# Optimization experiments

Hardware: AMD Instinct MI355X
Metric: run time of the kernel (lower is better)

Reference implementation:

```python
import jax, jax.numpy as jnp
import numpy as np

SCORE_THRESHOLD = 0.01
NMS_THRESHOLD = 0.5
MAX_DETECTIONS = 100
PRE_NMS_TOPK = 200  # candidates kept per class before NMS (>= MAX_DETECTIONS)


def setup_inputs() -> dict:
    key = jax.random.key(0)
    kc, kcls, kw, kr, kt = jax.random.split(key, 5)
    B, N, C, R = 16, 100000, 30, 3
    # Build valid (x1,y1,x2,y2) boxes: random centers in a 512x512 image, sizes in [1,101].
    cxy = jax.random.uniform(kc, (B, N, 2), dtype=jnp.float32) * 512.0
    wh = jax.random.uniform(kw, (B, N, 2), dtype=jnp.float32) * 100.0 + 1.0
    boxes = jnp.concatenate([cxy - 0.5 * wh, cxy + 0.5 * wh], axis=-1)  # [B,N,4]
    classification = jax.random.uniform(kcls, (B, N, C), dtype=jnp.float32)
    rotation = jax.random.normal(kr, (B, N, R), dtype=jnp.float32)
    translation = jax.random.normal(kt, (B, N, 3), dtype=jnp.float32)
    return {"boxes": boxes, "classification": classification,
            "rotation": rotation, "translation": translation}


def _iou_matrix(b):  # b: [K,4] -> [K,K] pairwise IoU
    x1, y1, x2, y2 = b[:, 0], b[:, 1], b[:, 2], b[:, 3]
    area = jnp.maximum(x2 - x1, 0.0) * jnp.maximum(y2 - y1, 0.0)
    xx1 = jnp.maximum(x1[:, None], x1[None, :])
    yy1 = jnp.maximum(y1[:, None], y1[None, :])
    xx2 = jnp.minimum(x2[:, None], x2[None, :])
    yy2 = jnp.minimum(y2[:, None], y2[None, :])
    inter = jnp.maximum(xx2 - xx1, 0.0) * jnp.maximum(yy2 - yy1, 0.0)
    union = area[:, None] + area[None, :] - inter
    return inter / jnp.maximum(union, 1e-8)


def _nms_one_class(scores, boxes):
    # scores: [N], boxes: [N,4] -> (kept_scores [K], source_indices [K])
    masked = jnp.where(scores > SCORE_THRESHOLD, scores, -jnp.inf)
    top_s, top_i = jax.lax.top_k(masked, PRE_NMS_TOPK)
    cand = boxes[top_i]                      # [K,4], already sorted by score desc
    iou = _iou_matrix(cand)                  # [K,K]
    valid = jnp.isfinite(top_s)
    rng = jnp.arange(PRE_NMS_TOPK)

    def body(i, keep):
        suppress = (iou[i] > NMS_THRESHOLD) & (rng > i) & keep[i]
        return keep & ~suppress

    keep = jax.lax.fori_loop(0, PRE_NMS_TOPK, body, valid)
    return jnp.where(keep, top_s, -jnp.inf), top_i


def reference(boxes, classification, rotation, translation):
    B, N, C = classification.shape

    def per_image(bx, cls, rot, tr):
        # Per-class score threshold + NMS, vectorized over classes.
        s, idx = jax.vmap(lambda c: _nms_one_class(cls[:, c], bx))(jnp.arange(C))
        labels = jnp.broadcast_to(jnp.arange(C)[:, None], s.shape)
        s, idx, labels = s.reshape(-1), idx.reshape(-1), labels.reshape(-1)
        # Global top-k over all (class, kept-box) pairs.
        top_s, sel = jax.lax.top_k(s, MAX_DETECTIONS)
        fidx, flab = idx[sel], labels[sel]
        valid = jnp.isfinite(top_s)
        out_boxes = jnp.where(valid[:, None], bx[fidx], -1.0)
        out_scores = jnp.where(valid, top_s, -1.0)
        out_labels = jnp.where(valid, flab, -1).astype(jnp.int32)
        out_rot = jnp.where(valid[:, None], rot[fidx], -1.0)
        out_tr = jnp.where(valid[:, None], tr[fidx], -1.0)
        return out_boxes, out_scores, out_labels, out_rot, out_tr

    return jax.vmap(per_image)(boxes, classification, rotation, translation)
```

## Files before the change

kernel.cpp:

```cpp
#include <hip/hip_runtime.h>
#include <math.h>

typedef unsigned long long u64;

#define BATCH 16
#define NBOX 100000
#define NCLS 30
#define K 200
#define MAXDET 100
#define SCORE_THR 0.01f
#define NMS_THR 0.5f
#define T0 0.995f

#define ELEM_PER_BATCH (NBOX * NCLS)
#define CAP 1024
#define CHUNKS 48
#define VEC_PER_CHUNK 15625
#define SEG 48
#define OVF 1000000

#define OFF_COLL   0ull
#define OFF_PCNT   (OFF_COLL + (size_t)BATCH*NCLS*CHUNKS*SEG*8)
#define OFF_WSI    (OFF_PCNT + (size_t)BATCH*CHUNKS*32*4)
#define OFF_MERGE  (OFF_WSI + (size_t)BATCH*NCLS*K*4)

__global__ __launch_bounds__(512) void collect_kernel(const float* __restrict__ cls,
                                                      int* __restrict__ pcnt,
                                                      u64* __restrict__ coll) {
  const int b = blockIdx.x / CHUNKS;
  const int chunk = blockIdx.x % CHUNKS;
  const int tid = threadIdx.x;

  __shared__ u64 lbuf[NCLS][SEG];
  __shared__ int lcnt[NCLS];

  if (tid < NCLS) lcnt[tid] = 0;
  __syncthreads();

  const int vbase = chunk * VEC_PER_CHUNK;
  const float4* p = (const float4*)(cls + (size_t)b * ELEM_PER_BATCH) + vbase;

  auto process = [&](float4 v, int idx) {
    float m = fmaxf(fmaxf(v.x, v.y), fmaxf(v.z, v.w));
    if (m > T0) {
      float vv[4] = {v.x, v.y, v.z, v.w};
      #pragma unroll
      for (int j = 0; j < 4; ++j) {
        if (vv[j] > T0) {
          int e = (vbase + idx) * 4 + j;
          int c = e % NCLS;
          int n = e / NCLS;
          int pos = atomicAdd(&lcnt[c], 1);
          if (pos < SEG)
            lbuf[c][pos] = ((u64)__float_as_uint(vv[j]) << 32) | (unsigned)(~(unsigned)n);
        }
      }
    }
  };

  int i = tid;
  for (; i + 1536 < VEC_PER_CHUNK; i += 2048) {
    float4 a  = p[i];
    float4 b2 = p[i + 512];
    float4 c2 = p[i + 1024];
    float4 d2 = p[i + 1536];
    process(a,  i);
    process(b2, i + 512);
    process(c2, i + 1024);
    process(d2, i + 1536);
  }
  for (; i < VEC_PER_CHUNK; i += 512) process(p[i], i);
  __syncthreads();

  if (tid < NCLS) {
    int m = lcnt[tid];
    pcnt[(b * CHUNKS + chunk) * 32 + tid] = (m > SEG) ? OVF : m;
    lcnt[tid] = (m < SEG) ? m : SEG;
  }
  __syncthreads();

  for (int t = tid; t < NCLS * SEG; t += 512) {
    int c = t / SEG, s = t - (t / SEG) * SEG;
    if (s < lcnt[c])
      coll[((size_t)(b * NCLS + c) * CHUNKS + chunk) * SEG + s] = lbuf[c][s];
  }
}

__global__ __launch_bounds__(512) void fused_sort_nms_kernel(
    const u64* __restrict__ coll, const int* __restrict__ pcnt,
    const float* __restrict__ cls, const float* __restrict__ boxes,
    int* __restrict__ ws_i, u64* __restrict__ merged) {
  const int bc = blockIdx.x;
  const int b = bc / NCLS, c = bc % NCLS;
  const int tid = threadIdx.x;

  __shared__ u64 arr[CAP];
  __shared__ u64 arr2[CAP];
  __shared__ float sx1[K], sy1[K], sx2[K], sy2[K], sarea[K], ss[K];
  __shared__ int sidx[K];
  __shared__ unsigned mask[K][8];
  __shared__ unsigned keepw[8];
  __shared__ int s_surv;
  __shared__ u64 comb[256];
  __shared__ unsigned eqbuf[512];
  __shared__ unsigned s_pref, s_mask, s_krem, s_takeall;
  __shared__ unsigned s_cntgt, s_cnteq;
  __shared__ int scnt[CHUNKS], soff[CHUNKS];
  __shared__ int s_total, s_bad;

  if (tid < CHUNKS) scnt[tid] = pcnt[(b * CHUNKS + tid) * 32 + c];
  __syncthreads();
  if (tid == 0) {
    int tot = 0, bad = 0;
    for (int ch = 0; ch < CHUNKS; ++ch) {
      int v = scnt[ch];
      if (v > SEG) bad = 1;
      soff[ch] = tot;
      tot += v;
    }
    if (tot < K || tot > CAP) bad = 1;
    s_total = tot; s_bad = bad;
  }
  __syncthreads();
  const bool bad = (s_bad != 0);

  if (!bad) {
    const int N = (s_total <= 512) ? 512 : CAP;
    for (int i = tid; i < N; i += 512) arr[i] = 0ull;
    __syncthreads();
    for (int t = tid; t < CHUNKS * SEG; t += 512) {
      int ch = t / SEG, s = t - (t / SEG) * SEG;
      if (s < scnt[ch])
        arr[soff[ch] + s] = coll[((size_t)bc * CHUNKS + ch) * SEG + s];
    }
    __syncthreads();

    {
      const int lane = tid & 63, w = tid >> 6;
      for (int run = w; run < (N >> 6); run += 8) {
        u64 v = arr[(run << 6) + lane];
        #pragma unroll
        for (int k = 2; k <= 64; k <<= 1) {
          #pragma unroll
          for (int j = k >> 1; j > 0; j >>= 1) {
            u64 o = __shfl_xor(v, j, 64);
            bool up = ((lane & k) == 0);
            bool lower = ((lane & j) == 0);
            u64 mn = (v < o) ? v : o;
            u64 mx = (v < o) ? o : v;
            v = (up != lower) ? mn : mx;
          }
        }
        arr[(run << 6) + lane] = v;
      }
    }
    __syncthreads();

    u64* src = arr;
    u64* dst = arr2;
    for (int L = 64; L < N; L <<= 1) {
      const int twoL = L << 1;
      for (int t = tid; t < N; t += 512) {
        int pair = t / twoL;
        int diag = t - pair * twoL;
        const u64* A = src + pair * twoL;
        const u64* B = A + L;
        int lo = (diag > L) ? (diag - L) : 0;
        int hi = (diag < L) ? diag : L;
        while (lo < hi) {
          int mid = (lo + hi) >> 1;
          if (A[mid] >= B[diag - 1 - mid]) lo = mid + 1; else hi = mid;
        }
        int i2 = lo, j2 = diag - lo;
        u64 av = (i2 < L) ? A[i2] : 0ull;
        u64 bv = (j2 < L) ? B[j2] : 0ull;
        dst[t] = (i2 < L && (j2 >= L || av >= bv)) ? av : bv;
      }
      __syncthreads();
      u64* tmp = src; src = dst; dst = tmp;
    }

    for (int r = tid; r < K; r += 512) {
      u64 e = src[r];
      float s = (e != 0ull) ? __uint_as_float((unsigned)(e >> 32)) : -INFINITY;
      int idx = (e != 0ull) ? (int)(~(unsigned)e) : 0;
      ss[r] = s; sidx[r] = idx;
      ws_i[bc * K + r] = idx;
    }
  } else {
    unsigned (*hist)[256] = (unsigned (*)[256])arr;
    const int wv = tid >> 6;
    if (tid == 0) { s_pref = 0u; s_mask = 0u; s_krem = K; s_takeall = 0u; }
    __syncthreads();
    const float* col = cls + (size_t)b * NBOX * NCLS + c;

    for (int pass = 0; pass < 4; ++pass) {
      if (s_takeall) break;
      const int shift = 24 - 8 * pass;
      for (int i = tid; i < 8 * 256; i += 512) ((unsigned*)hist)[i] = 0u;
      __syncthreads();
      const unsigned pref = s_pref, msk = s_mask;
      for (int n = tid; n < NBOX; n += 512) {
        float v = col[(size_t)n * NCLS];
        if (v > SCORE_THR) {
          unsigned key = __float_as_uint(v);
          if ((key & msk) == pref)
            atomicAdd(&hist[wv][(key >> shift) & 0xFFu], 1u);
        }
      }
      __syncthreads();
      if (tid < 256) {
        unsigned t2 = 0;
        for (int w = 0; w < 8; ++w) t2 += hist[w][tid];
        hist[0][tid] = t2;
      }
      __syncthreads();
      if (tid == 0) {
        unsigned krem = s_krem, cum = 0; int dsel = -1;
        for (int d = 255; d >= 0; --d) {
          unsigned cc = hist[0][d];
          if (cum + cc >= krem) { dsel = d; break; }
          cum += cc;
        }
        if (dsel < 0) s_takeall = 1u;
        else {
          s_krem = krem - cum;
          s_pref = pref | ((unsigned)dsel << shift);
          s_mask = msk | (0xFFu << shift);
        }
      }
      __syncthreads();
    }

    if (tid == 0) { s_cntgt = 0u; s_cnteq = 0u; }
    __syncthreads();
    const unsigned pivot = s_pref;
    const unsigned takeall = s_takeall;

    for (int n = tid; n < NBOX; n += 512) {
      float v = col[(size_t)n * NCLS];
      if (v > SCORE_THR) {
        unsigned key = __float_as_uint(v);
        if (takeall || key > pivot) {
          unsigned pos = atomicAdd(&s_cntgt, 1u);
          if (pos < 256u)
            comb[pos] = ((u64)key << 32) | (unsigned)(~(unsigned)n);
        } else if (key == pivot) {
          unsigned pos = atomicAdd(&s_cnteq, 1u);
          if (pos < 512u) eqbuf[pos] = (unsigned)n;
        }
      }
    }
    __syncthreads();
    const unsigned cntgt = (s_cntgt < 256u) ? s_cntgt : 256u;
    const unsigned cnteq = (s_cnteq < 512u) ? s_cnteq : 512u;
    unsigned need = 0;
    if (!takeall) {
      need = (cntgt < (unsigned)K) ? ((unsigned)K - cntgt) : 0u;
      if (need > cnteq) need = cnteq;
    }
    for (int i = tid; i < 512; i += 512)
      if ((unsigned)i >= cnteq) eqbuf[i] = 0xFFFFFFFFu;
    for (int k = 2; k <= 512; k <<= 1) {
      for (int j = k >> 1; j > 0; j >>= 1) {
        __syncthreads();
        {
          int i = tid, l = i ^ j;
          if (l > i) {
            unsigned a = eqbuf[i], bb = eqbuf[l];
            bool up = ((i & k) == 0);
            if (up ? (a > bb) : (a < bb)) { eqbuf[i] = bb; eqbuf[l] = a; }
          }
        }
      }
    }
    __syncthreads();
    for (int t = tid; t < (int)need; t += 512)
      comb[cntgt + t] = ((u64)pivot << 32) | (unsigned)(~eqbuf[t]);
    const unsigned M = cntgt + need;
    for (int i = tid; i < 256; i += 512)
      if ((unsigned)i >= M) comb[i] = 0ull;
    for (int k = 2; k <= 256; k <<= 1) {
      for (int j = k >> 1; j > 0; j >>= 1) {
        __syncthreads();
        if (tid < 256) {
          int i = tid, l = i ^ j;
          if (l > i) {
            u64 a = comb[i], bb = comb[l];
            bool up = ((i & k) == 0);
            if (up ? (a < bb) : (a > bb)) { comb[i] = bb; comb[l] = a; }
          }
        }
      }
    }
    __syncthreads();
    if (tid < K) {
      if ((unsigned)tid < M) {
        u64 e = comb[tid];
        ss[tid] = __uint_as_float((unsigned)(e >> 32));
        sidx[tid] = (int)(~(unsigned)e);
      } else {
        ss[tid] = -INFINITY;
        sidx[tid] = 0;
      }
      ws_i[bc * K + tid] = sidx[tid];
    }
  }
  for (int i = tid; i < K * 8; i += 512) ((unsigned*)mask)[i] = 0u;
  if (tid < 8) keepw[tid] = 0u;
  __syncthreads();

  for (int r = tid; r < K; r += 512) {
    float s = ss[r];
    bool valid = (s != -INFINITY);
    float x1 = 0.f, y1 = 0.f, x2 = 0.f, y2 = 0.f;
    if (valid) {
      const float* bp = boxes + ((size_t)b * NBOX + sidx[r]) * 4;
      x1 = bp[0]; y1 = bp[1]; x2 = bp[2]; y2 = bp[3];
      atomicOr(&keepw[r >> 5], 1u << (r & 31));
    }
    sx1[r] = x1; sy1[r] = y1; sx2[r] = x2; sy2[r] = y2;
    sarea[r] = fmaxf(x2 - x1, 0.f) * fmaxf(y2 - y1, 0.f);
  }
  __syncthreads();

  for (int t = tid; t < K * K; t += 512) {
    int i = t / K, j = t - i * K;
    if (j > i) {
      float xx1 = fmaxf(sx1[i], sx1[j]);
      float yy1 = fmaxf(sy1[i], sy1[j]);
      float xx2 = fminf(sx2[i], sx2[j]);
      float yy2 = fminf(sy2[i], sy2[j]);
      float inter = fmaxf(xx2 - xx1, 0.f) * fmaxf(yy2 - yy1, 0.f);
      float uni = sarea[i] + sarea[j] - inter;
      float iou = inter / fmaxf(uni, 1e-8f);
      if (iou > NMS_THR) atomicOr(&mask[i][j >> 5], 1u << (j & 31));
    }
  }
  __syncthreads();

  if (tid < 64) {
    int w = tid & 7;
    unsigned keep = keepw[w];
    for (int i = 0; i < K; ++i) {
      unsigned kw = __shfl(keep, i >> 5, 64);
      if ((kw >> (i & 31)) & 1u)
        keep &= ~mask[i][w];
    }
    if (tid < 8) keepw[tid] = keep;
  }
  __syncthreads();

  for (int r = tid; r < K; r += 512) {
    int w6 = r >> 5, bit = r & 31;
    if ((keepw[w6] >> bit) & 1u) {
      int pos = 0;
      #pragma unroll
      for (int w = 0; w < 7; ++w) {
        unsigned kw = keepw[w];
        if (w < w6) pos += __popc(kw);
        else if (w == w6) pos += __popc(kw & ((1u << bit) - 1u));
      }
      if (pos < 128) {
        unsigned ord = __float_as_uint(ss[r]) | 0x80000000u;
        merged[((size_t)b * 32 + c) * 128 + pos] =
          ((u64)ord << 32) | (unsigned)(~(unsigned)(c * K + r));
      }
    }
  }
  if (tid == 0) {
    int S = 0;
    #pragma unroll
    for (int w = 0; w < 7; ++w) S += __popc(keepw[w]);
    s_surv = S;
  }
  __syncthreads();
  for (int t = s_surv + tid; t < 128; t += 512)
    merged[((size_t)b * 32 + c) * 128 + t] = 0ull;
}

__device__ __forceinline__ int merge_path_128(const u64* __restrict__ A,
                                              const u64* __restrict__ B, int diag) {
  int lo = 0, hi = diag;
  while (lo < hi) {
    int mid = (lo + hi) >> 1;
    if (A[mid] >= B[diag - 1 - mid]) lo = mid + 1; else hi = mid;
  }
  return lo;
}

__global__ __launch_bounds__(1024) void merge_gather_kernel(
    const u64* __restrict__ merged, const int* __restrict__ ws_i,
    const float* __restrict__ boxes, const float* __restrict__ rot,
    const float* __restrict__ tr, float* __restrict__ out) {
  const int b = blockIdx.x;
  const int tid = threadIdx.x;
  __shared__ u64 S0[32 * 128];
  __shared__ u64 S1[16 * 128];

  for (int t = tid; t < 4096; t += 1024) {
    int c = t >> 7, r = t & 127;
    S0[t] = (c < NCLS) ? merged[((size_t)b * 32 + c) * 128 + r] : 0ull;
  }
  __syncthreads();

  #pragma unroll
  for (int level = 0; level < 5; ++level) {
    const int npairs = 16 >> level;
    const int nout = npairs * 128;
    const u64* src = (level & 1) ? S1 : S0;
    u64* dst = (level & 1) ? S0 : S1;
    for (int t = tid; t < nout; t += 1024) {
      int p = t >> 7, r = t & 127;
      const u64* A = src + (2 * p) * 128;
      const u64* B = src + (2 * p + 1) * 128;
      int i = merge_path_128(A, B, r);
      int j = r - i;
      u64 a = A[i], bb = B[j];
      dst[p * 128 + r] = (a >= bb) ? a : bb;
    }
    __syncthreads();
  }

  if (tid < MAXDET) {
    u64 key = S1[tid];
    bool valid = (key != 0ull);
    float* ob  = out + ((size_t)b * MAXDET + tid) * 4;
    float* os  = out + (size_t)BATCH * MAXDET * 4 + b * MAXDET + tid;
    float* ol  = os + BATCH * MAXDET;
    float* orr = out + (size_t)BATCH * MAXDET * 6 + ((size_t)b * MAXDET + tid) * 3;
    float* ot  = orr + (size_t)BATCH * MAXDET * 3;

    if (valid) {
      unsigned f = ~(unsigned)key;
      int cl = (int)(f / K);
      float sc = __uint_as_float((unsigned)(key >> 32) & 0x7FFFFFFFu);
      int orig = ws_i[(size_t)b * NCLS * K + f];
      const float* bp = boxes + ((size_t)b * NBOX + orig) * 4;
      ob[0] = bp[0]; ob[1] = bp[1]; ob[2] = bp[2]; ob[3] = bp[3];
      *os = sc;
      *ol = (float)cl;
      const float* rp = rot + ((size_t)b * NBOX + orig) * 3;
      orr[0] = rp[0]; orr[1] = rp[1]; orr[2] = rp[2];
      const float* tp = tr + ((size_t)b * NBOX + orig) * 3;
      ot[0] = tp[0]; ot[1] = tp[1]; ot[2] = tp[2];
    } else {
      ob[0] = ob[1] = ob[2] = ob[3] = -1.f;
      *os = -1.f; *ol = -1.f;
      orr[0] = orr[1] = orr[2] = -1.f;
      ot[0] = ot[1] = ot[2] = -1.f;
    }
  }
}

extern "C" void kernel_launch(void* const* d_in, const int* in_sizes, int n_in,
                              void* d_out, int out_size, void* d_ws, size_t ws_size,
                              hipStream_t stream) {
  const float* boxes = (const float*)d_in[0];
  const float* cls   = (const float*)d_in[1];
  const float* rot   = (const float*)d_in[2];
  const float* tr    = (const float*)d_in[3];
  float* out = (float*)d_out;

  char* ws = (char*)d_ws;
  u64*   coll   = (u64*)(ws + OFF_COLL);
  int*   pcnt   = (int*)(ws + OFF_PCNT);
  int*   ws_i   = (int*)(ws + OFF_WSI);
  u64*   merged = (u64*)(ws + OFF_MERGE);

  collect_kernel<<<BATCH * CHUNKS, 512, 0, stream>>>(cls, pcnt, coll);
  fused_sort_nms_kernel<<<BATCH * NCLS, 512, 0, stream>>>(coll, pcnt, cls, boxes,
                                                          ws_i, merged);
  merge_gather_kernel<<<BATCH, 1024, 0, stream>>>(merged, ws_i, boxes, rot, tr, out);
}
```

Before: 92.98 us.

## Fuse three kernels into one cooperative kernel with grid-wide syncs

Merges the collect, per-class sort+NMS, and final merge/gather kernels into a single cooperative kernel of BATCH*NCLS blocks, separated by grid.sync() barriers. The collect phase is re-chunked to 30 chunks of 25000 vectors with 64-entry segments so the collect grid matches the per-class block count. This is meant to remove kernel launch gaps and inter-kernel drain. In exchange it adds grid-barrier cost, caps occupancy through launch bounds, and gives the collect phase fewer, larger blocks.

```diff
diff --git a/kernel.cpp b/kernel.cpp
--- a/kernel.cpp
+++ b/kernel.cpp
@@ -1,6 +1,8 @@
 #include <hip/hip_runtime.h>
+#include <hip/hip_cooperative_groups.h>
 #include <math.h>
 
+namespace cg = cooperative_groups;
 typedef unsigned long long u64;
 
 #define BATCH 16
@@ -14,88 +16,28 @@
 
 #define ELEM_PER_BATCH (NBOX * NCLS)
 #define CAP 1024
-#define CHUNKS 48
-#define VEC_PER_CHUNK 15625
-#define SEG 48
+#define CHUNKS 30
+#define VEC_PER_CHUNK 25000
+#define SEG 64
 #define OVF 1000000
+#define NBLK (BATCH * NCLS)
 
 #define OFF_COLL   0ull
-#define OFF_PCNT   (OFF_COLL + (size_t)BATCH*NCLS*CHUNKS*SEG*8)
-#define OFF_WSI    (OFF_PCNT + (size_t)BATCH*CHUNKS*32*4)
-#define OFF_MERGE  (OFF_WSI + (size_t)BATCH*NCLS*K*4)
-
-__global__ __launch_bounds__(512) void collect_kernel(const float* __restrict__ cls,
-                                                      int* __restrict__ pcnt,
-                                                      u64* __restrict__ coll) {
-  const int b = blockIdx.x / CHUNKS;
-  const int chunk = blockIdx.x % CHUNKS;
+#define OFF_PCNT   (OFF_COLL + (size_t)NBLK*CHUNKS*SEG*8)
+#define OFF_WSI    (OFF_PCNT + (size_t)NBLK*32*4)
+#define OFF_MERGE  (OFF_WSI + (size_t)NBLK*K*4)
+
+__global__ __launch_bounds__(512, 4) void mega_kernel(
+    const float* __restrict__ cls, const float* __restrict__ boxes,
+    const float* __restrict__ rot, const float* __restrict__ tr,
+    int* __restrict__ pcnt, u64* __restrict__ coll,
+    int* __restrict__ ws_i, u64* __restrict__ merged, float* __restrict__ out) {
+  cg::grid_group grid = cg::this_grid();
+  const int blk = blockIdx.x;
   const int tid = threadIdx.x;
 
-  __shared__ u64 lbuf[NCLS][SEG];
-  __shared__ int lcnt[NCLS];
-
-  if (tid < NCLS) lcnt[tid] = 0;
-  __syncthreads();
-
-  const int vbase = chunk * VEC_PER_CHUNK;
-  const float4* p = (const float4*)(cls + (size_t)b * ELEM_PER_BATCH) + vbase;
-
-  auto process = [&](float4 v, int idx) {
-    float m = fmaxf(fmaxf(v.x, v.y), fmaxf(v.z, v.w));
-    if (m > T0) {
-      float vv[4] = {v.x, v.y, v.z, v.w};
-      #pragma unroll
-      for (int j = 0; j < 4; ++j) {
-        if (vv[j] > T0) {
-          int e = (vbase + idx) * 4 + j;
-          int c = e % NCLS;
-          int n = e / NCLS;
-          int pos = atomicAdd(&lcnt[c], 1);
-          if (pos < SEG)
-            lbuf[c][pos] = ((u64)__float_as_uint(vv[j]) << 32) | (unsigned)(~(unsigned)n);
-        }
-      }
-    }
-  };
-
-  int i = tid;
-  for (; i + 1536 < VEC_PER_CHUNK; i += 2048) {
-    float4 a  = p[i];
-    float4 b2 = p[i + 512];
-    float4 c2 = p[i + 1024];
-    float4 d2 = p[i + 1536];
-    process(a,  i);
-    process(b2, i + 512);
-    process(c2, i + 1024);
-    process(d2, i + 1536);
-  }
-  for (; i < VEC_PER_CHUNK; i += 512) process(p[i], i);
-  __syncthreads();
-
-  if (tid < NCLS) {
-    int m = lcnt[tid];
-    pcnt[(b * CHUNKS + chunk) * 32 + tid] = (m > SEG) ? OVF : m;
-    lcnt[tid] = (m < SEG) ? m : SEG;
-  }
-  __syncthreads();
-
-  for (int t = tid; t < NCLS * SEG; t += 512) {
-    int c = t / SEG, s = t - (t / SEG) * SEG;
-    if (s < lcnt[c])
-      coll[((size_t)(b * NCLS + c) * CHUNKS + chunk) * SEG + s] = lbuf[c][s];
-  }
-}
-
-__global__ __launch_bounds__(512) void fused_sort_nms_kernel(
-    const u64* __restrict__ coll, const int* __restrict__ pcnt,
-    const float* __restrict__ cls, const float* __restrict__ boxes,
-    int* __restrict__ ws_i, u64* __restrict__ merged) {
-  const int bc = blockIdx.x;
-  const int b = bc / NCLS, c = bc % NCLS;
-  const int tid = threadIdx.x;
-
-  __shared__ u64 arr[CAP];
-  __shared__ u64 arr2[CAP];
+  __shared__ u64 bufA[4096];
+  __shared__ u64 S1[2048];
   __shared__ float sx1[K], sy1[K], sx2[K], sy2[K], sarea[K], ss[K];
   __shared__ int sidx[K];
   __shared__ unsigned mask[K][8];
@@ -105,350 +47,405 @@
   __shared__ unsigned eqbuf[512];
   __shared__ unsigned s_pref, s_mask, s_krem, s_takeall;
   __shared__ unsigned s_cntgt, s_cnteq;
+  __shared__ int lcnt[NCLS];
   __shared__ int scnt[CHUNKS], soff[CHUNKS];
   __shared__ int s_total, s_bad;
 
-  if (tid < CHUNKS) scnt[tid] = pcnt[(b * CHUNKS + tid) * 32 + c];
-  __syncthreads();
-  if (tid == 0) {
-    int tot = 0, bad = 0;
-    for (int ch = 0; ch < CHUNKS; ++ch) {
-      int v = scnt[ch];
-      if (v > SEG) bad = 1;
-      soff[ch] = tot;
-      tot += v;
-    }
-    if (tot < K || tot > CAP) bad = 1;
-    s_total = tot; s_bad = bad;
+  {
+    const int b = blk / CHUNKS, chunk = blk % CHUNKS;
+    u64 (*lbuf)[SEG] = (u64 (*)[SEG])bufA;
+
+    if (tid < NCLS) lcnt[tid] = 0;
+    __syncthreads();
+
+    const int vbase = chunk * VEC_PER_CHUNK;
+    const float4* p = (const float4*)(cls + (size_t)b * ELEM_PER_BATCH) + vbase;
+
+    auto process = [&](float4 v, int idx) {
+      float m = fmaxf(fmaxf(v.x, v.y), fmaxf(v.z, v.w));
+      if (m > T0) {
+        float vv[4] = {v.x, v.y, v.z, v.w};
+        #pragma unroll
+        for (int j = 0; j < 4; ++j) {
+          if (vv[j] > T0) {
+            int e = (vbase + idx) * 4 + j;
+            int c = e % NCLS;
+            int n = e / NCLS;
+            int pos = atomicAdd(&lcnt[c], 1);
+            if (pos < SEG)
+              lbuf[c][pos] = ((u64)__float_as_uint(vv[j]) << 32) | (unsigned)(~(unsigned)n);
+          }
+        }
+      }
+    };
+
+    int i = tid;
+    for (; i + 1536 < VEC_PER_CHUNK; i += 2048) {
+      float4 a  = p[i];
+      float4 b2 = p[i + 512];
+      float4 c2 = p[i + 1024];
+      float4 d2 = p[i + 1536];
+      process(a,  i);
+      process(b2, i + 512);
+      process(c2, i + 1024);
+      process(d2, i + 1536);
+    }
+    for (; i < VEC_PER_CHUNK; i += 512) process(p[i], i);
+    __syncthreads();
+
+    if (tid < NCLS) {
+      int m = lcnt[tid];
+      pcnt[(b * CHUNKS + chunk) * 32 + tid] = (m > SEG) ? OVF : m;
+      lcnt[tid] = (m < SEG) ? m : SEG;
+    }
+    __syncthreads();
+
+    for (int t = tid; t < NCLS * SEG; t += 512) {
+      int c = t >> 6, s = t & (SEG - 1);
+      if (s < lcnt[c])
+        coll[((size_t)(b * NCLS + c) * CHUNKS + chunk) * SEG + s] = lbuf[c][s];
+    }
   }
-  __syncthreads();
-  const bool bad = (s_bad != 0);
-
-  if (!bad) {
-    const int N = (s_total <= 512) ? 512 : CAP;
-    for (int i = tid; i < N; i += 512) arr[i] = 0ull;
-    __syncthreads();
-    for (int t = tid; t < CHUNKS * SEG; t += 512) {
-      int ch = t / SEG, s = t - (t / SEG) * SEG;
-      if (s < scnt[ch])
-        arr[soff[ch] + s] = coll[((size_t)bc * CHUNKS + ch) * SEG + s];
-    }
-    __syncthreads();
-
-    {
-      const int lane = tid & 63, w = tid >> 6;
-      for (int run = w; run < (N >> 6); run += 8) {
-        u64 v = arr[(run << 6) + lane];
-        #pragma unroll
-        for (int k = 2; k <= 64; k <<= 1) {
+  grid.sync();
+
+  {
+    const int bc = blk;
+    const int b = bc / NCLS, c = bc % NCLS;
+    u64* arr  = bufA;
+    u64* arr2 = bufA + 1024;
+
+    if (tid < CHUNKS) scnt[tid] = pcnt[(b * CHUNKS + tid) * 32 + c];
+    __syncthreads();
+    if (tid == 0) {
+      int tot = 0, bad = 0;
+      for (int ch = 0; ch < CHUNKS; ++ch) {
+        int v = scnt[ch];
+        if (v > SEG) bad = 1;
+        soff[ch] = tot;
+        tot += v;
+      }
+      if (tot < K || tot > CAP) bad = 1;
+      s_total = tot; s_bad = bad;
+    }
+    __syncthreads();
+    const bool bad = (s_bad != 0);
+
+    if (!bad) {
+      const int N = (s_total <= 512) ? 512 : CAP;
+      for (int i = tid; i < N; i += 512) arr[i] = 0ull;
+      __syncthreads();
+      for (int t = tid; t < CHUNKS * SEG; t += 512) {
+        int ch = t >> 6, s = t & (SEG - 1);
+        if (s < scnt[ch])
+          arr[soff[ch] + s] = coll[((size_t)bc * CHUNKS + ch) * SEG + s];
+      }
+      __syncthreads();
+
+      {
+        const int lane = tid & 63, w = tid >> 6;
+        for (int run = w; run < (N >> 6); run += 8) {
+          u64 v = arr[(run << 6) + lane];
           #pragma unroll
-          for (int j = k >> 1; j > 0; j >>= 1) {
-            u64 o = __shfl_xor(v, j, 64);
-            bool up = ((lane & k) == 0);
-            bool lower = ((lane & j) == 0);
-            u64 mn = (v < o) ? v : o;
-            u64 mx = (v < o) ? o : v;
-            v = (up != lower) ? mn : mx;
-          }
-        }
-        arr[(run << 6) + lane] = v;
-      }
-    }
-    __syncthreads();
-
-    u64* src = arr;
-    u64* dst = arr2;
-    for (int L = 64; L < N; L <<= 1) {
-      const int twoL = L << 1;
-      for (int t = tid; t < N; t += 512) {
-        int pair = t / twoL;
-        int diag = t - pair * twoL;
-        const u64* A = src + pair * twoL;
-        const u64* B = A + L;
-        int lo = (diag > L) ? (diag - L) : 0;
-        int hi = (diag < L) ? diag : L;
-        while (lo < hi) {
-          int mid = (lo + hi) >> 1;
-          if (A[mid] >= B[diag - 1 - mid]) lo = mid + 1; else hi = mid;
-        }
-        int i2 = lo, j2 = diag - lo;
-        u64 av = (i2 < L) ? A[i2] : 0ull;
-        u64 bv = (j2 < L) ? B[j2] : 0ull;
-        dst[t] = (i2 < L && (j2 >= L || av >= bv)) ? av : bv;
-      }
-      __syncthreads();
-      u64* tmp = src; src = dst; dst = tmp;
-    }
-
-    for (int r = tid; r < K; r += 512) {
-      u64 e = src[r];
-      float s = (e != 0ull) ? __uint_as_float((unsigned)(e >> 32)) : -INFINITY;
-      int idx = (e != 0ull) ? (int)(~(unsigned)e) : 0;
-      ss[r] = s; sidx[r] = idx;
-      ws_i[bc * K + r] = idx;
-    }
-  } else {
-    unsigned (*hist)[256] = (unsigned (*)[256])arr;
-    const int wv = tid >> 6;
-    if (tid == 0) { s_pref = 0u; s_mask = 0u; s_krem = K; s_takeall = 0u; }
-    __syncthreads();
-    const float* col = cls + (size_t)b * NBOX * NCLS + c;
-
-    for (int pass = 0; pass < 4; ++pass) {
-      if (s_takeall) break;
-      const int shift = 24 - 8 * pass;
-      for (int i = tid; i < 8 * 256; i += 512) ((unsigned*)hist)[i] = 0u;
-      __syncthreads();
-      const unsigned pref = s_pref, msk = s_mask;
+          for (int k = 2; k <= 64; k <<= 1) {
+            #pragma unroll
+            for (int j = k >> 1; j > 0; j >>= 1) {
+              u64 o = __shfl_xor(v, j, 64);
+              bool up = ((lane & k) == 0);
+              bool lower = ((lane & j) == 0);
+              u64 mn = (v < o) ? v : o;
+              u64 mx = (v < o) ? o : v;
+              v = (up != lower) ? mn : mx;
+            }
+          }
+          arr[(run << 6) + lane] = v;
+        }
+      }
+      __syncthreads();
+
+      u64* src = arr;
+      u64* dst = arr2;
+      for (int L = 64; L < N; L <<= 1) {
+        const int twoL = L << 1;
+        for (int t = tid; t < N; t += 512) {
+          int pair = t / twoL;
+          int diag = t - pair * twoL;
+          const u64* A = src + pair * twoL;
+          const u64* B = A + L;
+          int lo = (diag > L) ? (diag - L) : 0;
+          int hi = (diag < L) ? diag : L;
+          while (lo < hi) {
+            int mid = (lo + hi) >> 1;
+            if (A[mid] >= B[diag - 1 - mid]) lo = mid + 1; else hi = mid;
+          }
+          int i2 = lo, j2 = diag - lo;
+          u64 av = (i2 < L) ? A[i2] : 0ull;
+          u64 bv = (j2 < L) ? B[j2] : 0ull;
+          dst[t] = (i2 < L && (j2 >= L || av >= bv)) ? av : bv;
+        }
+        __syncthreads();
+        u64* tmp = src; src = dst; dst = tmp;
+      }
+
+      for (int r = tid; r < K; r += 512) {
+        u64 e = src[r];
+        float s = (e != 0ull) ? __uint_as_float((unsigned)(e >> 32)) : -INFINITY;
+        int idx = (e != 0ull) ? (int)(~(unsigned)e) : 0;
+        ss[r] = s; sidx[r] = idx;
+        ws_i[bc * K + r] = idx;
+      }
+    } else {
+      unsigned (*hist)[256] = (unsigned (*)[256])bufA;
+      const int wv = tid >> 6;
+      if (tid == 0) { s_pref = 0u; s_mask = 0u; s_krem = K; s_takeall = 0u; }
+      __syncthreads();
+      const float* col = cls + (size_t)b * NBOX * NCLS + c;
+
+      for (int pass = 0; pass < 4; ++pass) {
+        if (s_takeall) break;
+        const int shift = 24 - 8 * pass;
+        for (int i = tid; i < 8 * 256; i += 512) ((unsigned*)hist)[i] = 0u;
+        __syncthreads();
+        const unsigned pref = s_pref, msk = s_mask;
+        for (int n = tid; n < NBOX; n += 512) {
+          float v = col[(size_t)n * NCLS];
+          if (v > SCORE_THR) {
+            unsigned key = __float_as_uint(v);
+            if ((key & msk) == pref)
+              atomicAdd(&hist[wv][(key >> shift) & 0xFFu], 1u);
+          }
+        }
+        __syncthreads();
+        if (tid < 256) {
+          unsigned t2 = 0;
+          for (int w = 0; w < 8; ++w) t2 += hist[w][tid];
+          hist[0][tid] = t2;
+        }
+        __syncthreads();
+        if (tid == 0) {
+          unsigned krem = s_krem, cum = 0; int dsel = -1;
+          for (int d = 255; d >= 0; --d) {
+            unsigned cc = hist[0][d];
+            if (cum + cc >= krem) { dsel = d; break; }
+            cum += cc;
+          }
+          if (dsel < 0) s_takeall = 1u;
+          else {
+            s_krem = krem - cum;
+            s_pref = pref | ((unsigned)dsel << shift);
+            s_mask = msk | (0xFFu << shift);
+          }
+        }
+        __syncthreads();
+      }
+
+      if (tid == 0) { s_cntgt = 0u; s_cnteq = 0u; }
+      __syncthreads();
+      const unsigned pivot = s_pref;
+      const unsigned takeall = s_takeall;
+
       for (int n = tid; n < NBOX; n += 512) {
         float v = col[(size_t)n * NCLS];
         if (v > SCORE_THR) {
           unsigned key = __float_as_uint(v);
-          if ((key & msk) == pref)
-            atomicAdd(&hist[wv][(key >> shift) & 0xFFu], 1u);
-        }
-      }
-      __syncthreads();
-      if (tid < 256) {
-        unsigned t2 = 0;
-        for (int w = 0; w < 8; ++w) t2 += hist[w][tid];
-        hist[0][tid] = t2;
-      }
-      __syncthreads();
-      if (tid == 0) {
-        unsigned krem = s_krem, cum = 0; int dsel = -1;
-        for (int d = 255; d >= 0; --d) {
-          unsigned cc = hist[0][d];
-          if (cum + cc >= krem) { dsel = d; break; }
-          cum += cc;
-        }
-        if (dsel < 0) s_takeall = 1u;
-        else {
-          s_krem = krem - cum;
-          s_pref = pref | ((unsigned)dsel << shift);
-          s_mask = msk | (0xFFu << shift);
-        }
-      }
-      __syncthreads();
-    }
-
-    if (tid == 0) { s_cntgt = 0u; s_cnteq = 0u; }
-    __syncthreads();
-    const unsigned pivot = s_pref;
-    const unsigned takeall = s_takeall;
-
-    for (int n = tid; n < NBOX; n += 512) {
-      float v = col[(size_t)n * NCLS];
-      if (v > SCORE_THR) {
-        unsigned key = __float_as_uint(v);
-        if (takeall || key > pivot) {
-          unsigned pos = atomicAdd(&s_cntgt, 1u);
-          if (pos < 256u)
-            comb[pos] = ((u64)key << 32) | (unsigned)(~(unsigned)n);
-        } else if (key == pivot) {
-          unsigned pos = atomicAdd(&s_cnteq, 1u);
-          if (pos < 512u) eqbuf[pos] = (unsigned)n;
-        }
-      }
-    }
-    __syncthreads();
-    const unsigned cntgt = (s_cntgt < 256u) ? s_cntgt : 256u;
-    const unsigned cnteq = (s_cnteq < 512u) ? s_cnteq : 512u;
-    unsigned need = 0;
-    if (!takeall) {
-      need = (cntgt < (unsigned)K) ? ((unsigned)K - cntgt) : 0u;
-      if (need > cnteq) need = cnteq;
-    }
-    for (int i = tid; i < 512; i += 512)
-      if ((unsigned)i >= cnteq) eqbuf[i] = 0xFFFFFFFFu;
-    for (int k = 2; k <= 512; k <<= 1) {
-      for (int j = k >> 1; j > 0; j >>= 1) {
-        __syncthreads();
-        {
-          int i = tid, l = i ^ j;
-          if (l > i) {
-            unsigned a = eqbuf[i], bb = eqbuf[l];
-            bool up = ((i & k) == 0);
-            if (up ? (a > bb) : (a < bb)) { eqbuf[i] = bb; eqbuf[l] = a; }
-          }
-        }
-      }
-    }
-    __syncthreads();
-    for (int t = tid; t < (int)need; t += 512)
-      comb[cntgt + t] = ((u64)pivot << 32) | (unsigned)(~eqbuf[t]);
-    const unsigned M = cntgt + need;
-    for (int i = tid; i < 256; i += 512)
-      if ((unsigned)i >= M) comb[i] = 0ull;
-    for (int k = 2; k <= 256; k <<= 1) {
-      for (int j = k >> 1; j > 0; j >>= 1) {
-        __syncthreads();
-        if (tid < 256) {
-          int i = tid, l = i ^ j;
-          if (l > i) {
-            u64 a = comb[i], bb = comb[l];
-            bool up = ((i & k) == 0);
-            if (up ? (a < bb) : (a > bb)) { comb[i] = bb; comb[l] = a; }
-          }
-        }
-      }
-    }
-    __syncthreads();
-    if (tid < K) {
-      if ((unsigned)tid < M) {
-        u64 e = comb[tid];
-        ss[tid] = __uint_as_float((unsigned)(e >> 32));
-        sidx[tid] = (int)(~(unsigned)e);
+          if (takeall || key > pivot) {
+            unsigned pos = atomicAdd(&s_cntgt, 1u);
+            if (pos < 256u)
+              comb[pos] = ((u64)key << 32) | (unsigned)(~(unsigned)n);
+          } else if (key == pivot) {
+            unsigned pos = atomicAdd(&s_cnteq, 1u);
+            if (pos < 512u) eqbuf[pos] = (unsigned)n;
+          }
+        }
+      }
+      __syncthreads();
+      const unsigned cntgt = (s_cntgt < 256u) ? s_cntgt : 256u;
+      const unsigned cnteq = (s_cnteq < 512u) ? s_cnteq : 512u;
+      unsigned need = 0;
+      if (!takeall) {
+        need = (cntgt < (unsigned)K) ? ((unsigned)K - cntgt) : 0u;
+        if (need > cnteq) need = cnteq;
+      }
+      for (int i = tid; i < 512; i += 512)
+        if ((unsigned)i >= cnteq) eqbuf[i] = 0xFFFFFFFFu;
+      for (int k = 2; k <= 512; k <<= 1) {
+        for (int j = k >> 1; j > 0; j >>= 1) {
+          __syncthreads();
+          {
+            int i = tid, l = i ^ j;
+            if (l > i) {
+              unsigned a = eqbuf[i], bb = eqbuf[l];
+              bool up = ((i & k) == 0);
+              if (up ? (a > bb) : (a < bb)) { eqbuf[i] = bb; eqbuf[l] = a; }
+            }
+          }
+        }
+      }
+      __syncthreads();
+      for (int t = tid; t < (int)need; t += 512)
+        comb[cntgt + t] = ((u64)pivot << 32) | (unsigned)(~eqbuf[t]);
+      const unsigned M = cntgt + need;
+      for (int i = tid; i < 256; i += 512)
+        if ((unsigned)i >= M) comb[i] = 0ull;
+      for (int k = 2; k <= 256; k <<= 1) {
+        for (int j = k >> 1; j > 0; j >>= 1) {
+          __syncthreads();
+          if (tid < 256) {
+            int i = tid, l = i ^ j;
+            if (l > i) {
+              u64 a = comb[i], bb = comb[l];
+              bool up = ((i & k) == 0);
+              if (up ? (a < bb) : (a > bb)) { comb[i] = bb; comb[l] = a; }
+            }
+          }
+        }
+      }
+      __syncthreads();
+      if (tid < K) {
+        if ((unsigned)tid < M) {
+          u64 e = comb[tid];
+          ss[tid] = __uint_as_float((unsigned)(e >> 32));
+          sidx[tid] = (int)(~(unsigned)e);
+        } else {
+          ss[tid] = -INFINITY;
+          sidx[tid] = 0;
+        }
+        ws_i[bc * K + tid] = sidx[tid];
+      }
+    }
+    for (int i = tid; i < K * 8; i += 512) ((unsigned*)mask)[i] = 0u;
+    if (tid < 8) keepw[tid] = 0u;
+    __syncthreads();
+
+    for (int r = tid; r < K; r += 512) {
+      float s = ss[r];
+      bool valid = (s != -INFINITY);
+      float x1 = 0.f, y1 = 0.f, x2 = 0.f, y2 = 0.f;
+      if (valid) {
+        const float* bp = boxes + ((size_t)b * NBOX + sidx[r]) * 4;
+        x1 = bp[0]; y1 = bp[1]; x2 = bp[2]; y2 = bp[3];
+        atomicOr(&keepw[r >> 5], 1u << (r & 31));
+      }
+      sx1[r] = x1; sy1[r] = y1; sx2[r] = x2; sy2[r] = y2;
+      sarea[r] = fmaxf(x2 - x1, 0.f) * fmaxf(y2 - y1, 0.f);
+    }
+    __syncthreads();
+
+    for (int t = tid; t < K * K; t += 512) {
+      int i = t / K, j = t - i * K;
+      if (j > i) {
+        float xx1 = fmaxf(sx1[i], sx1[j]);
+        float yy1 = fmaxf(sy1[i], sy1[j]);
+        float xx2 = fminf(sx2[i], sx2[j]);
+        float yy2 = fminf(sy2[i], sy2[j]);
+        float inter = fmaxf(xx2 - xx1, 0.f) * fmaxf(yy2 - yy1, 0.f);
+        float uni = sarea[i] + sarea[j] - inter;
+        float iou = inter / fmaxf(uni, 1e-8f);
+        if (iou > NMS_THR) atomicOr(&mask[i][j >> 5], 1u << (j & 31));
+      }
+    }
+    __syncthreads();
+
+    if (tid < 64) {
+      int w = tid & 7;
+      unsigned keep = keepw[w];
+      for (int i = 0; i < K; ++i) {
+        unsigned kw = __shfl(keep, i >> 5, 64);
+        if ((kw >> (i & 31)) & 1u)
+          keep &= ~mask[i][w];
+      }
+      if (tid < 8) keepw[tid] = keep;
+    }
+    __syncthreads();
+
+    for (int r = tid; r < K; r += 512) {
+      int w6 = r >> 5, bit = r & 31;
+      if ((keepw[w6] >> bit) & 1u) {
+        int pos = 0;
+        #pragma unroll
+        for (int w = 0; w < 7; ++w) {
+          unsigned kw = keepw[w];
+          if (w < w6) pos += __popc(kw);
+          else if (w == w6) pos += __popc(kw & ((1u << bit) - 1u));
+        }
+        if (pos < 128) {
+          unsigned ord = __float_as_uint(ss[r]) | 0x80000000u;
+          merged[((size_t)b * 32 + c) * 128 + pos] =
+            ((u64)ord << 32) | (unsigned)(~(unsigned)(c * K + r));
+        }
+      }
+    }
+    if (tid == 0) {
+      int S = 0;
+      #pragma unroll
+      for (int w = 0; w < 7; ++w) S += __popc(keepw[w]);
+      s_surv = S;
+    }
+    __syncthreads();
+    for (int t = s_surv + tid; t < 128; t += 512)
+      merged[((size_t)b * 32 + c) * 128 + t] = 0ull;
+  }
+  grid.sync();
+
+  if (blk < BATCH) {
+    const int b = blk;
+    u64* S0 = bufA;
+
+    for (int t = tid; t < 4096; t += 512) {
+      int c = t >> 7, r = t & 127;
+      S0[t] = (c < NCLS) ? merged[((size_t)b * 32 + c) * 128 + r] : 0ull;
+    }
+    __syncthreads();
+
+    #pragma unroll
+    for (int level = 0; level < 5; ++level) {
+      const int npairs = 16 >> level;
+      const int nout = npairs * 128;
+      const u64* src = (level & 1) ? S1 : S0;
+      u64* dst = (level & 1) ? S0 : S1;
+      for (int t = tid; t < nout; t += 512) {
+        int p = t >> 7, r = t & 127;
+        const u64* A = src + (2 * p) * 128;
+        const u64* B = src + (2 * p + 1) * 128;
+        int lo = 0, hi = r;
+        while (lo < hi) {
+          int mid = (lo + hi) >> 1;
+          if (A[mid] >= B[r - 1 - mid]) lo = mid + 1; else hi = mid;
+        }
+        int i = lo, j = r - i;
+        u64 a = A[i], bb = B[j];
+        dst[p * 128 + r] = (a >= bb) ? a : bb;
+      }
+      __syncthreads();
+    }
+
+    if (tid < MAXDET) {
+      u64 key = S1[tid];
+      bool valid = (key != 0ull);
+      float* ob  = out + ((size_t)b * MAXDET + tid) * 4;
+      float* os  = out + (size_t)BATCH * MAXDET * 4 + b * MAXDET + tid;
+      float* ol  = os + BATCH * MAXDET;
+      float* orr = out + (size_t)BATCH * MAXDET * 6 + ((size_t)b * MAXDET + tid) * 3;
+      float* ot  = orr + (size_t)BATCH * MAXDET * 3;
+
+      if (valid) {
+        unsigned f = ~(unsigned)key;
+        int cl = (int)(f / K);
+        float sc = __uint_as_float((unsigned)(key >> 32) & 0x7FFFFFFFu);
+        int orig = ws_i[(size_t)b * NCLS * K + f];
+        const float* bp = boxes + ((size_t)b * NBOX + orig) * 4;
+        ob[0] = bp[0]; ob[1] = bp[1]; ob[2] = bp[2]; ob[3] = bp[3];
+        *os = sc;
+        *ol = (float)cl;
+        const float* rp = rot + ((size_t)b * NBOX + orig) * 3;
+        orr[0] = rp[0]; orr[1] = rp[1]; orr[2] = rp[2];
+        const float* tp = tr + ((size_t)b * NBOX + orig) * 3;
+        ot[0] = tp[0]; ot[1] = tp[1]; ot[2] = tp[2];
       } else {
-        ss[tid] = -INFINITY;
-        sidx[tid] = 0;
-      }
-      ws_i[bc * K + tid] = sidx[tid];
-    }
-  }
-  for (int i = tid; i < K * 8; i += 512) ((unsigned*)mask)[i] = 0u;
-  if (tid < 8) keepw[tid] = 0u;
-  __syncthreads();
-
-  for (int r = tid; r < K; r += 512) {
-    float s = ss[r];
-    bool valid = (s != -INFINITY);
-    float x1 = 0.f, y1 = 0.f, x2 = 0.f, y2 = 0.f;
-    if (valid) {
-      const float* bp = boxes + ((size_t)b * NBOX + sidx[r]) * 4;
-      x1 = bp[0]; y1 = bp[1]; x2 = bp[2]; y2 = bp[3];
-      atomicOr(&keepw[r >> 5], 1u << (r & 31));
-    }
-    sx1[r] = x1; sy1[r] = y1; sx2[r] = x2; sy2[r] = y2;
-    sarea[r] = fmaxf(x2 - x1, 0.f) * fmaxf(y2 - y1, 0.f);
-  }
-  __syncthreads();
-
-  for (int t = tid; t < K * K; t += 512) {
-    int i = t / K, j = t - i * K;
-    if (j > i) {
-      float xx1 = fmaxf(sx1[i], sx1[j]);
-      float yy1 = fmaxf(sy1[i], sy1[j]);
-      float xx2 = fminf(sx2[i], sx2[j]);
-      float yy2 = fminf(sy2[i], sy2[j]);
-      float inter = fmaxf(xx2 - xx1, 0.f) * fmaxf(yy2 - yy1, 0.f);
-      float uni = sarea[i] + sarea[j] - inter;
-      float iou = inter / fmaxf(uni, 1e-8f);
-      if (iou > NMS_THR) atomicOr(&mask[i][j >> 5], 1u << (j & 31));
-    }
-  }
-  __syncthreads();
-
-  if (tid < 64) {
-    int w = tid & 7;
-    unsigned keep = keepw[w];
-    for (int i = 0; i < K; ++i) {
-      unsigned kw = __shfl(keep, i >> 5, 64);
-      if ((kw >> (i & 31)) & 1u)
-        keep &= ~mask[i][w];
-    }
-    if (tid < 8) keepw[tid] = keep;
-  }
-  __syncthreads();
-
-  for (int r = tid; r < K; r += 512) {
-    int w6 = r >> 5, bit = r & 31;
-    if ((keepw[w6] >> bit) & 1u) {
-      int pos = 0;
-      #pragma unroll
-      for (int w = 0; w < 7; ++w) {
-        unsigned kw = keepw[w];
-        if (w < w6) pos += __popc(kw);
-        else if (w == w6) pos += __popc(kw & ((1u << bit) - 1u));
-      }
-      if (pos < 128) {
-        unsigned ord = __float_as_uint(ss[r]) | 0x80000000u;
-        merged[((size_t)b * 32 + c) * 128 + pos] =
-          ((u64)ord << 32) | (unsigned)(~(unsigned)(c * K + r));
-      }
-    }
-  }
-  if (tid == 0) {
-    int S = 0;
-    #pragma unroll
-    for (int w = 0; w < 7; ++w) S += __popc(keepw[w]);
-    s_surv = S;
-  }
-  __syncthreads();
-  for (int t = s_surv + tid; t < 128; t += 512)
-    merged[((size_t)b * 32 + c) * 128 + t] = 0ull;
-}
-
-__device__ __forceinline__ int merge_path_128(const u64* __restrict__ A,
-                                              const u64* __restrict__ B, int diag) {
-  int lo = 0, hi = diag;
-  while (lo < hi) {
-    int mid = (lo + hi) >> 1;
-    if (A[mid] >= B[diag - 1 - mid]) lo = mid + 1; else hi = mid;
-  }
-  return lo;
-}
-
-__global__ __launch_bounds__(1024) void merge_gather_kernel(
-    const u64* __restrict__ merged, const int* __restrict__ ws_i,
-    const float* __restrict__ boxes, const float* __restrict__ rot,
-    const float* __restrict__ tr, float* __restrict__ out) {
-  const int b = blockIdx.x;
-  const int tid = threadIdx.x;
-  __shared__ u64 S0[32 * 128];
-  __shared__ u64 S1[16 * 128];
-
-  for (int t = tid; t < 4096; t += 1024) {
-    int c = t >> 7, r = t & 127;
-    S0[t] = (c < NCLS) ? merged[((size_t)b * 32 + c) * 128 + r] : 0ull;
-  }
-  __syncthreads();
-
-  #pragma unroll
-  for (int level = 0; level < 5; ++level) {
-    const int npairs = 16 >> level;
-    const int nout = npairs * 128;
-    const u64* src = (level & 1) ? S1 : S0;
-    u64* dst = (level & 1) ? S0 : S1;
-    for (int t = tid; t < nout; t += 1024) {
-      int p = t >> 7, r = t & 127;
-      const u64* A = src + (2 * p) * 128;
-      const u64* B = src + (2 * p + 1) * 128;
-      int i = merge_path_128(A, B, r);
-      int j = r - i;
-      u64 a = A[i], bb = B[j];
-      dst[p * 128 + r] = (a >= bb) ? a : bb;
-    }
-    __syncthreads();
-  }
-
-  if (tid < MAXDET) {
-    u64 key = S1[tid];
-    bool valid = (key != 0ull);
-    float* ob  = out + ((size_t)b * MAXDET + tid) * 4;
-    float* os  = out + (size_t)BATCH * MAXDET * 4 + b * MAXDET + tid;
-    float* ol  = os + BATCH * MAXDET;
-    float* orr = out + (size_t)BATCH * MAXDET * 6 + ((size_t)b * MAXDET + tid) * 3;
-    float* ot  = orr + (size_t)BATCH * MAXDET * 3;
-
-    if (valid) {
-      unsigned f = ~(unsigned)key;
-      int cl = (int)(f / K);
-      float sc = __uint_as_float((unsigned)(key >> 32) & 0x7FFFFFFFu);
-      int orig = ws_i[(size_t)b * NCLS * K + f];
-      const float* bp = boxes + ((size_t)b * NBOX + orig) * 4;
-      ob[0] = bp[0]; ob[1] = bp[1]; ob[2] = bp[2]; ob[3] = bp[3];
-      *os = sc;
-      *ol = (float)cl;
-      const float* rp = rot + ((size_t)b * NBOX + orig) * 3;
-      orr[0] = rp[0]; orr[1] = rp[1]; orr[2] = rp[2];
-      const float* tp = tr + ((size_t)b * NBOX + orig) * 3;
-      ot[0] = tp[0]; ot[1] = tp[1]; ot[2] = tp[2];
-    } else {
-      ob[0] = ob[1] = ob[2] = ob[3] = -1.f;
-      *os = -1.f; *ol = -1.f;
-      orr[0] = orr[1] = orr[2] = -1.f;
-      ot[0] = ot[1] = ot[2] = -1.f;
+        ob[0] = ob[1] = ob[2] = ob[3] = -1.f;
+        *os = -1.f; *ol = -1.f;
+        orr[0] = orr[1] = orr[2] = -1.f;
+        ot[0] = ot[1] = ot[2] = -1.f;
+      }
     }
   }
 }
@@ -463,13 +460,14 @@
   float* out = (float*)d_out;
 
   char* ws = (char*)d_ws;
-  u64*   coll   = (u64*)(ws + OFF_COLL);
-  int*   pcnt   = (int*)(ws + OFF_PCNT);
-  int*   ws_i   = (int*)(ws + OFF_WSI);
-  u64*   merged = (u64*)(ws + OFF_MERGE);
-
-  collect_kernel<<<BATCH * CHUNKS, 512, 0, stream>>>(cls, pcnt, coll);
-  fused_sort_nms_kernel<<<BATCH * NCLS, 512, 0, stream>>>(coll, pcnt, cls, boxes,
-                                                          ws_i, merged);
-  merge_gather_kernel<<<BATCH, 1024, 0, stream>>>(merged, ws_i, boxes, rot, tr, out);
+  u64* coll   = (u64*)(ws + OFF_COLL);
+  int* pcnt   = (int*)(ws + OFF_PCNT);
+  int* ws_i   = (int*)(ws + OFF_WSI);
+  u64* merged = (u64*)(ws + OFF_MERGE);
+
+  void* args[] = {(void*)&cls, (void*)&boxes, (void*)&rot, (void*)&tr,
+                  (void*)&pcnt, (void*)&coll, (void*)&ws_i, (void*)&merged,
+                  (void*)&out};
+  hipLaunchCooperativeKernel((const void*)mega_kernel, dim3(NBLK), dim3(512),
+                             args, 0, stream);
 }
```

Measured after the change: 183.4 us. +97.3%, slower.

## Build NMS suppression mask with wavefront ballots and scalarize the keep-mask scan

Applied to the files above, without the earlier changes.

The IoU mask is now built by giving each thread a fixed column j and looping over rows i. Each wavefront writes a 64-bit ballot word straight into the mask, so the shared-memory atomicOr calls, the integer division and the mask zeroing pass are gone. The sequential suppression scan keeps all seven keep words in registers and applies each row with a branchless select read through vectorized uint4 loads, instead of a per-lane shuffle loop. Every row and word is now computed, including the lower triangle, so the mask is fully written. Some extra IoU work is done in exchange for removing atomic contention and divergence.

```diff
diff --git a/kernel.cpp b/kernel.cpp
--- a/kernel.cpp
+++ b/kernel.cpp
@@ -306,7 +306,7 @@
       ws_i[bc * K + tid] = sidx[tid];
     }
   }
-  for (int i = tid; i < K * 8; i += 512) ((unsigned*)mask)[i] = 0u;
+
   if (tid < 8) keepw[tid] = 0u;
   __syncthreads();
 
@@ -324,30 +324,64 @@
   }
   __syncthreads();
 
-  for (int t = tid; t < K * K; t += 512) {
-    int i = t / K, j = t - i * K;
-    if (j > i) {
-      float xx1 = fmaxf(sx1[i], sx1[j]);
-      float yy1 = fmaxf(sy1[i], sy1[j]);
-      float xx2 = fminf(sx2[i], sx2[j]);
-      float yy2 = fminf(sy2[i], sy2[j]);
+  {
+    const int jj = tid & 255;
+    const bool jv = (jj < K);
+    float jx1 = 0.f, jy1 = 0.f, jx2 = 0.f, jy2 = 0.f, ja = 0.f;
+    if (jv) {
+      jx1 = sx1[jj]; jy1 = sy1[jj]; jx2 = sx2[jj]; jy2 = sy2[jj]; ja = sarea[jj];
+    }
+    const int wordbase = ((tid & 255) >> 6) * 2;
+    const int g = tid >> 8;
+    for (int k2 = 0; k2 < K / 2; ++k2) {
+      int i = g + 2 * k2;
+      float ix1 = sx1[i], iy1 = sy1[i], ix2 = sx2[i], iy2 = sy2[i], ia = sarea[i];
+      float xx1 = fmaxf(ix1, jx1);
+      float yy1 = fmaxf(iy1, jy1);
+      float xx2 = fminf(ix2, jx2);
+      float yy2 = fminf(iy2, jy2);
       float inter = fmaxf(xx2 - xx1, 0.f) * fmaxf(yy2 - yy1, 0.f);
-      float uni = sarea[i] + sarea[j] - inter;
+      float uni = ia + ja - inter;
       float iou = inter / fmaxf(uni, 1e-8f);
-      if (iou > NMS_THR) atomicOr(&mask[i][j >> 5], 1u << (j & 31));
+      bool sup = jv && (jj > i) && (iou > NMS_THR);
+      u64 bal = __ballot(sup);
+      if ((tid & 63) == 0)
+        *(u64*)&mask[i][wordbase] = bal;
     }
   }
   __syncthreads();
 
   if (tid < 64) {
-    int w = tid & 7;
-    unsigned keep = keepw[w];
-    for (int i = 0; i < K; ++i) {
-      unsigned kw = __shfl(keep, i >> 5, 64);
-      if ((kw >> (i & 31)) & 1u)
-        keep &= ~mask[i][w];
-    }
-    if (tid < 8) keepw[tid] = keep;
+    unsigned k0 = keepw[0], k1 = keepw[1], k2_ = keepw[2], k3 = keepw[3];
+    unsigned k4 = keepw[4], k5 = keepw[5], k6 = keepw[6];
+#define NMS_ROW(I, KW, B)                                              \
+    {                                                                  \
+      unsigned sel = (unsigned)0 - ((KW >> (B)) & 1u);                 \
+      const uint4 ma = *(const uint4*)&mask[I][0];                     \
+      const uint4 mb = *(const uint4*)&mask[I][4];                     \
+      k0 &= ~(ma.x & sel); k1 &= ~(ma.y & sel);                        \
+      k2_ &= ~(ma.z & sel); k3 &= ~(ma.w & sel);                       \
+      k4 &= ~(mb.x & sel); k5 &= ~(mb.y & sel); k6 &= ~(mb.z & sel);   \
+    }
+    #pragma unroll 8
+    for (int bq = 0; bq < 32; ++bq) NMS_ROW(bq, k0, bq)
+    #pragma unroll 8
+    for (int bq = 0; bq < 32; ++bq) NMS_ROW(32 + bq, k1, bq)
+    #pragma unroll 8
+    for (int bq = 0; bq < 32; ++bq) NMS_ROW(64 + bq, k2_, bq)
+    #pragma unroll 8
+    for (int bq = 0; bq < 32; ++bq) NMS_ROW(96 + bq, k3, bq)
+    #pragma unroll 8
+    for (int bq = 0; bq < 32; ++bq) NMS_ROW(128 + bq, k4, bq)
+    #pragma unroll 8
+    for (int bq = 0; bq < 32; ++bq) NMS_ROW(160 + bq, k5, bq)
+    #pragma unroll 8
+    for (int bq = 0; bq < 8; ++bq) NMS_ROW(192 + bq, k6, bq)
+#undef NMS_ROW
+    if (tid == 0) {
+      keepw[0] = k0; keepw[1] = k1; keepw[2] = k2_; keepw[3] = k3;
+      keepw[4] = k4; keepw[5] = k5; keepw[6] = k6;
+    }
   }
   __syncthreads();
 
```

After: 95.53 us. 1.03x slower.

## Fuse per-image merge/gather into NMS kernel via last-block atomic counter

Applied to the files above, without the earlier changes.

Removes the separate merge_gather kernel launch. Each (batch,class) NMS block now increments a per-batch atomic counter after writing its survivors, and the last block to finish for an image performs the cross-class merge and output gather. The counter is zeroed in the collect kernel. This saves a kernel launch and its dependency gap. In exchange it enlarges the shared memory footprint of the NMS kernel, which may lower occupancy, and the merge now runs with 512 threads instead of 1024.

```diff
diff --git a/kernel.cpp b/kernel.cpp
--- a/kernel.cpp
+++ b/kernel.cpp
@@ -21,15 +21,19 @@
 
 #define OFF_COLL   0ull
 #define OFF_PCNT   (OFF_COLL + (size_t)BATCH*NCLS*CHUNKS*SEG*8)
-#define OFF_WSI    (OFF_PCNT + (size_t)BATCH*CHUNKS*32*4)
+#define OFF_BCNT   (OFF_PCNT + (size_t)BATCH*CHUNKS*32*4)
+#define OFF_WSI    (OFF_BCNT + 64*4)
 #define OFF_MERGE  (OFF_WSI + (size_t)BATCH*NCLS*K*4)
 
 __global__ __launch_bounds__(512) void collect_kernel(const float* __restrict__ cls,
                                                       int* __restrict__ pcnt,
-                                                      u64* __restrict__ coll) {
+                                                      u64* __restrict__ coll,
+                                                      int* __restrict__ bcnt) {
   const int b = blockIdx.x / CHUNKS;
   const int chunk = blockIdx.x % CHUNKS;
   const int tid = threadIdx.x;
+
+  if (blockIdx.x == 0 && tid < BATCH) bcnt[tid] = 0;
 
   __shared__ u64 lbuf[NCLS][SEG];
   __shared__ int lcnt[NCLS];
@@ -89,18 +93,21 @@
 __global__ __launch_bounds__(512) void fused_sort_nms_kernel(
     const u64* __restrict__ coll, const int* __restrict__ pcnt,
     const float* __restrict__ cls, const float* __restrict__ boxes,
-    int* __restrict__ ws_i, u64* __restrict__ merged) {
+    const float* __restrict__ rot, const float* __restrict__ tr,
+    int* __restrict__ ws_i, u64* __restrict__ merged,
+    int* __restrict__ bcnt, float* __restrict__ out) {
   const int bc = blockIdx.x;
   const int b = bc / NCLS, c = bc % NCLS;
   const int tid = threadIdx.x;
 
-  __shared__ u64 arr[CAP];
-  __shared__ u64 arr2[CAP];
+  __shared__ u64 S[6144];
+  u64* arr  = S;
+  u64* arr2 = S + 1024;
   __shared__ float sx1[K], sy1[K], sx2[K], sy2[K], sarea[K], ss[K];
   __shared__ int sidx[K];
   __shared__ unsigned mask[K][8];
   __shared__ unsigned keepw[8];
-  __shared__ int s_surv;
+  __shared__ int s_surv, s_last;
   __shared__ u64 comb[256];
   __shared__ unsigned eqbuf[512];
   __shared__ unsigned s_pref, s_mask, s_krem, s_takeall;
@@ -369,38 +376,28 @@
     }
   }
   if (tid == 0) {
-    int S = 0;
+    int S2 = 0;
     #pragma unroll
-    for (int w = 0; w < 7; ++w) S += __popc(keepw[w]);
-    s_surv = S;
+    for (int w = 0; w < 7; ++w) S2 += __popc(keepw[w]);
+    s_surv = S2;
   }
   __syncthreads();
   for (int t = s_surv + tid; t < 128; t += 512)
     merged[((size_t)b * 32 + c) * 128 + t] = 0ull;
-}
-
-__device__ __forceinline__ int merge_path_128(const u64* __restrict__ A,
-                                              const u64* __restrict__ B, int diag) {
-  int lo = 0, hi = diag;
-  while (lo < hi) {
-    int mid = (lo + hi) >> 1;
-    if (A[mid] >= B[diag - 1 - mid]) lo = mid + 1; else hi = mid;
-  }
-  return lo;
-}
-
-__global__ __launch_bounds__(1024) void merge_gather_kernel(
-    const u64* __restrict__ merged, const int* __restrict__ ws_i,
-    const float* __restrict__ boxes, const float* __restrict__ rot,
-    const float* __restrict__ tr, float* __restrict__ out) {
-  const int b = blockIdx.x;
-  const int tid = threadIdx.x;
-  __shared__ u64 S0[32 * 128];
-  __shared__ u64 S1[16 * 128];
-
-  for (int t = tid; t < 4096; t += 1024) {
-    int c = t >> 7, r = t & 127;
-    S0[t] = (c < NCLS) ? merged[((size_t)b * 32 + c) * 128 + r] : 0ull;
+
+  __syncthreads();
+  __threadfence();
+  if (tid == 0)
+    s_last = (atomicAdd(&bcnt[b], 1) == NCLS - 1) ? 1 : 0;
+  __syncthreads();
+  if (!s_last) return;
+  __threadfence();
+
+  u64* S0 = S;
+  u64* S1 = S + 4096;
+  for (int t = tid; t < 4096; t += 512) {
+    int c2 = t >> 7, r = t & 127;
+    S0[t] = (c2 < NCLS) ? merged[((size_t)b * 32 + c2) * 128 + r] : 0ull;
   }
   __syncthreads();
 
@@ -410,12 +407,16 @@
     const int nout = npairs * 128;
     const u64* src = (level & 1) ? S1 : S0;
     u64* dst = (level & 1) ? S0 : S1;
-    for (int t = tid; t < nout; t += 1024) {
+    for (int t = tid; t < nout; t += 512) {
       int p = t >> 7, r = t & 127;
       const u64* A = src + (2 * p) * 128;
       const u64* B = src + (2 * p + 1) * 128;
-      int i = merge_path_128(A, B, r);
-      int j = r - i;
+      int lo = 0, hi = r;
+      while (lo < hi) {
+        int mid = (lo + hi) >> 1;
+        if (A[mid] >= B[r - 1 - mid]) lo = mid + 1; else hi = mid;
+      }
+      int i = lo, j = r - i;
       u64 a = A[i], bb = B[j];
       dst[p * 128 + r] = (a >= bb) ? a : bb;
     }
@@ -465,11 +466,12 @@
   char* ws = (char*)d_ws;
   u64*   coll   = (u64*)(ws + OFF_COLL);
   int*   pcnt   = (int*)(ws + OFF_PCNT);
+  int*   bcnt   = (int*)(ws + OFF_BCNT);
   int*   ws_i   = (int*)(ws + OFF_WSI);
   u64*   merged = (u64*)(ws + OFF_MERGE);
 
-  collect_kernel<<<BATCH * CHUNKS, 512, 0, stream>>>(cls, pcnt, coll);
+  collect_kernel<<<BATCH * CHUNKS, 512, 0, stream>>>(cls, pcnt, coll, bcnt);
   fused_sort_nms_kernel<<<BATCH * NCLS, 512, 0, stream>>>(coll, pcnt, cls, boxes,
-                                                          ws_i, merged);
-  merge_gather_kernel<<<BATCH, 1024, 0, stream>>>(merged, ws_i, boxes, rot, tr, out);
+                                                          rot, tr, ws_i, merged,
+                                                          bcnt, out);
 }
```

New measurement: 143.5 us. 1.54x slower.
